# Optimization experiments

Measured on AMD Instinct MI355X. Metric: run time of the kernel, lower is better.

Reference implementation:

```python
import jax, jax.numpy as jnp
import numpy as np

N = 100_000   # nodes
E = 1_600_000 # edges
IN = 128
OUT = 64
L = 3         # n_layers


def setup_inputs() -> dict:
    key = jax.random.key(0)
    ks = jax.random.split(key, 4)
    x = jax.random.normal(ks[0], (N, IN), dtype=jnp.float32)
    edge_index = jax.random.randint(ks[1], (2, E), 0, N, dtype=jnp.int64)
    # Glorot-ish init like torch Linear default
    s0 = 1.0 / np.sqrt(IN)
    W0 = jax.random.uniform(ks[2], (IN, OUT), jnp.float32, -s0, s0)
    b0 = jnp.zeros((OUT,), jnp.float32)
    so = 1.0 / np.sqrt(OUT)
    Ws = jax.random.uniform(ks[3], (L - 1, OUT, OUT), jnp.float32, -so, so)
    bs = jnp.zeros((L - 1, OUT), jnp.float32)
    return {"x": x, "edge_index": edge_index, "W0": W0, "b0": b0, "Ws": Ws, "bs": bs}


def _gcn_conv(x, src, dst, norm, W, b):
    # dense transform then degree-normalized scatter-add over edges (incl. self-loops)
    h = x @ W                                  # [N, out]
    msg = h[src] * norm[:, None]               # [E+N, out]
    out = jax.ops.segment_sum(msg, dst, num_segments=N)
    return out + b


def reference(x, edge_index, W0, b0, Ws, bs):
    loops = jnp.arange(N, dtype=edge_index.dtype)
    src = jnp.concatenate([edge_index[0], loops])  # source nodes (x_j)
    dst = jnp.concatenate([edge_index[1], loops])  # aggregation targets
    # symmetric GCN normalization: deg over A+I, norm = d^-1/2[src]*d^-1/2[dst]
    deg = jax.ops.segment_sum(jnp.ones(src.shape, x.dtype), dst, num_segments=N)
    dinv = jnp.where(deg > 0, jax.lax.rsqrt(deg), jnp.zeros((), x.dtype))
    norm = dinv[src] * dinv[dst]

    x_temp = _gcn_conv(x, src, dst, norm, W0, b0)
    h = x_temp
    for i in range(L - 1):  # fixed small layer loop
        h = jax.nn.relu(_gcn_conv(h, src, dst, norm, Ws[i], bs[i]))
    return h + x_temp  # sum_res residual
```

## Files before the change

### kernel.cpp

```cpp
#include <hip/hip_runtime.h>


#define LB 8
#define BKN 256
#define CHUNK 4096
#define EPT 16
#define SEPT 20
#define CAP 8192
#define PADS 3
#define CAPCOL (CAP + BKN * PADS)

typedef unsigned short ushort_t;
typedef __attribute__((ext_vector_type(8))) short bf16x8;
typedef __attribute__((ext_vector_type(4))) float f32x4;

__device__ __forceinline__ unsigned f2bf(float f) {
    unsigned u = __builtin_bit_cast(unsigned, f);
    return (u + 0x7FFFu + ((u >> 16) & 1u)) >> 16;
}
__device__ __forceinline__ float bflo(unsigned u) {
    return __builtin_bit_cast(float, u << 16);
}
__device__ __forceinline__ float bfhi(unsigned u) {
    return __builtin_bit_cast(float, u & 0xFFFF0000u);
}

__device__ int detect_f64(const int* ei, int E, int* sflag) {
    if (threadIdx.x == 0) *sflag = 0;
    __syncthreads();
    const unsigned* raw = (const unsigned*)ei;
    int dwords = min(2 * E, 512);
    int any = 0;
    for (int i = threadIdx.x; i < dwords; i += blockDim.x)
        if ((i & 1) && raw[i]) any = 1;
    if (any) atomicOr(sflag, 1);
    __syncthreads();
    return !*sflag;
}

__global__ __launch_bounds__(256) void k_scatter(
        const int* __restrict__ ei, int E,
        int* __restrict__ bucketCursor, unsigned int* __restrict__ packed) {
    __shared__ int hist[512];
    __shared__ int base[512];
    __shared__ int sflag;
    int f64 = detect_f64(ei, E, &sflag);
    int b0 = blockIdx.x * CHUNK;
    int n = min(CHUNK, E - b0);
    int tid = threadIdx.x;
    for (int i = tid; i < 512; i += 256) hist[i] = 0;
    __syncthreads();
    int dreg[EPT], sreg[EPT];
    bool vec_ok = f64 ? ((E & 1) == 0) : ((E & 3) == 0);
    if (vec_ok) {
#pragma unroll
        for (int j = 0; j < EPT / 4; j++) {
            int idx = tid * 4 + j * 1024;
            if (idx + 3 < n) {
                int e = b0 + idx;
                if (f64) {
                    uint4 sa = *(const uint4*)(ei + 2 * (size_t)e);
                    uint4 sb = *(const uint4*)(ei + 2 * (size_t)e + 4);
                    uint4 da = *(const uint4*)(ei + 2 * ((size_t)E + e));
                    uint4 db = *(const uint4*)(ei + 2 * ((size_t)E + e) + 4);
                    sreg[j * 4 + 0] = (int)sa.x; sreg[j * 4 + 1] = (int)sa.z;
                    sreg[j * 4 + 2] = (int)sb.x; sreg[j * 4 + 3] = (int)sb.z;
                    dreg[j * 4 + 0] = (int)da.x; dreg[j * 4 + 1] = (int)da.z;
                    dreg[j * 4 + 2] = (int)db.x; dreg[j * 4 + 3] = (int)db.z;
                } else {
                    uint4 sv = *(const uint4*)(ei + e);
                    uint4 dv = *(const uint4*)(ei + E + e);
                    sreg[j * 4 + 0] = (int)sv.x; sreg[j * 4 + 1] = (int)sv.y;
                    sreg[j * 4 + 2] = (int)sv.z; sreg[j * 4 + 3] = (int)sv.w;
                    dreg[j * 4 + 0] = (int)dv.x; dreg[j * 4 + 1] = (int)dv.y;
                    dreg[j * 4 + 2] = (int)dv.z; dreg[j * 4 + 3] = (int)dv.w;
                }
            } else {
#pragma unroll
                for (int k = 0; k < 4; k++) {
                    int ii = idx + k;
                    if (ii < n) {
                        int e = b0 + ii;
                        dreg[j * 4 + k] = f64 ? ei[2 * (E + e)] : ei[E + e];
                        sreg[j * 4 + k] = f64 ? ei[2 * e] : ei[e];
                    } else {
                        dreg[j * 4 + k] = -1;
                    }
                }
            }
        }
    } else {
#pragma unroll
        for (int i = 0; i < EPT; i++) {
            int idx = tid + i * 256;
            if (idx < n) {
                int e = b0 + idx;
                dreg[i] = f64 ? ei[2 * (E + e)] : ei[E + e];
                sreg[i] = f64 ? ei[2 * e] : ei[e];
            } else {
                dreg[i] = -1;
            }
        }
    }
#pragma unroll
    for (int i = 0; i < EPT; i++)
        if (dreg[i] >= 0) atomicAdd(&hist[dreg[i] >> LB], 1);
    __syncthreads();
    for (int i = tid; i < 512; i += 256) {
        int c = hist[i];
        base[i] = c ? atomicAdd(&bucketCursor[i], c) : 0;
        hist[i] = 0;
    }
    __syncthreads();
#pragma unroll
    for (int i = 0; i < EPT; i++) {
        if (dreg[i] >= 0) {
            int bk = dreg[i] >> LB;
            int pos = bk * CAP + base[bk] + atomicAdd(&hist[bk], 1);
            packed[pos] = ((unsigned)sreg[i] << LB) | (unsigned)(dreg[i] & (BKN - 1));
        }
    }
}

__global__ __launch_bounds__(256) void k_sort(
        const unsigned int* __restrict__ packed, const int* __restrict__ bucketCursor,
        int* __restrict__ col, int2* __restrict__ rp2, float* __restrict__ dinv,
        ushort_t* __restrict__ hs, int N) {
    __shared__ int hist[BKN];
    __shared__ int cur[BKN];
    __shared__ int wtot[4];
    int tid = threadIdx.x;
    int b = blockIdx.x;
    int start = b * CAP;
    int cnt = bucketCursor[b];
    int end = start + cnt;
    int inreg = (cnt <= 256 * SEPT);
    unsigned preg[SEPT];
    hist[tid] = 0;
    __syncthreads();
    if (inreg) {
#pragma unroll
        for (int i = 0; i < SEPT; i++) {
            int e = start + tid + i * 256;
            if (e < end) {
                preg[i] = packed[e];
                atomicAdd(&hist[preg[i] & (BKN - 1)], 1);
            }
        }
    } else {
        for (int e = start + tid; e < end; e += 256)
            atomicAdd(&hist[packed[e] & (BKN - 1)], 1);
    }
    __syncthreads();
    int v = hist[tid];
    int pv = (v + PADS) & ~PADS;
    int lane = tid & 63, wid = tid >> 6;
    int sc = pv;
#pragma unroll
    for (int off = 1; off < 64; off <<= 1) {
        int x = __shfl_up(sc, off);
        if (lane >= off) sc += x;
    }
    if (lane == 63) wtot[wid] = sc;
    __syncthreads();
    int add = 0;
#pragma unroll
    for (int w2 = 0; w2 < 3; w2++)
        if (wid > w2) add += wtot[w2];
    int excl = sc + add - pv;
    int st = b * CAPCOL + excl;
    cur[tid] = st;
    int node = (b << LB) + tid;
    if (node < N) {
        rp2[node] = make_int2(st, st + pv);
        dinv[node] = rsqrtf((float)(v + 1));
        for (int i = v; i < pv; i++) col[st + i] = N;
    }
    if (b == 0 && tid < 64) hs[(size_t)N * 64 + tid] = 0;
    __syncthreads();
    if (inreg) {
#pragma unroll
        for (int i = 0; i < SEPT; i++) {
            int e = start + tid + i * 256;
            if (e < end) {
                unsigned pvk = preg[i];
                int pos = atomicAdd(&cur[pvk & (BKN - 1)], 1);
                col[pos] = (int)(pvk >> LB);
            }
        }
    } else {
        for (int e = start + tid; e < end; e += 256) {
            unsigned pvk = packed[e];
            int pos = atomicAdd(&cur[pvk & (BKN - 1)], 1);
            col[pos] = (int)(pvk >> LB);
        }
    }
}

__global__ __launch_bounds__(256) void k_gemm1(
        const float* __restrict__ A, const float* __restrict__ W,
        const float* __restrict__ dinv, ushort_t* __restrict__ out, int nrows) {
    const int K = 128;
    __shared__ ushort_t sWT[64 * (K + 8)];
    int tid = threadIdx.x;
    for (int i = tid; i < K * 64; i += 256) {
        int n = i & 63, k = i >> 6;
        sWT[n * (K + 8) + k] = (ushort_t)f2bf(W[i]);
    }
    __syncthreads();
    int wave = tid >> 6, lane = tid & 63;
    int quad = lane >> 4, l16 = lane & 15;
    int rowBase = blockIdx.x * 128 + wave * 32;
    f32x4 acc[2][4];
#pragma unroll
    for (int r = 0; r < 2; r++)
#pragma unroll
        for (int c = 0; c < 4; c++) acc[r][c] = (f32x4){0.f, 0.f, 0.f, 0.f};
#pragma unroll
    for (int chunk = 0; chunk < K / 32; chunk++) {
        bf16x8 afr[2];
#pragma unroll
        for (int r = 0; r < 2; r++) {
            int row = rowBase + r * 16 + l16;
            if (row >= nrows) row = nrows - 1;
            const float* ap = A + (size_t)row * K + chunk * 32 + quad * 8;
            float4 v0 = *(const float4*)ap;
            float4 v1 = *(const float4*)(ap + 4);
            bf16x8 a;
            a[0] = (short)f2bf(v0.x); a[1] = (short)f2bf(v0.y);
            a[2] = (short)f2bf(v0.z); a[3] = (short)f2bf(v0.w);
            a[4] = (short)f2bf(v1.x); a[5] = (short)f2bf(v1.y);
            a[6] = (short)f2bf(v1.z); a[7] = (short)f2bf(v1.w);
            afr[r] = a;
        }
#pragma unroll
        for (int c = 0; c < 4; c++) {
            bf16x8 bfr = __builtin_bit_cast(
                bf16x8,
                *(const uint4*)&sWT[(c * 16 + l16) * (K + 8) + chunk * 32 + quad * 8]);
#pragma unroll
            for (int r = 0; r < 2; r++)
                acc[r][c] = __builtin_amdgcn_mfma_f32_16x16x32_bf16(
                    afr[r], bfr, acc[r][c], 0, 0, 0);
        }
    }
#pragma unroll
    for (int r = 0; r < 2; r++)
#pragma unroll
        for (int i = 0; i < 4; i++) {
            int row = rowBase + r * 16 + quad * 4 + i;
            if (row < nrows) {
                float sc = dinv[row];
#pragma unroll
                for (int c = 0; c < 4; c++)
                    out[(size_t)row * 64 + c * 16 + l16] =
                        (ushort_t)f2bf(acc[r][c][i] * sc);
            }
        }
}

__global__ __launch_bounds__(256) void k_gemm64(
        const ushort_t* __restrict__ A, const float* __restrict__ W,
        const float* __restrict__ dinv, ushort_t* __restrict__ out, int nrows) {
    const int K = 64;
    __shared__ ushort_t sWT[64 * (K + 8)];
    int tid = threadIdx.x;
    for (int i = tid; i < K * 64; i += 256) {
        int n = i & 63, k = i >> 6;
        sWT[n * (K + 8) + k] = (ushort_t)f2bf(W[i]);
    }
    __syncthreads();
    int wave = tid >> 6, lane = tid & 63;
    int quad = lane >> 4, l16 = lane & 15;
    int rowBase = blockIdx.x * 128 + wave * 32;
    f32x4 acc[2][4];
#pragma unroll
    for (int r = 0; r < 2; r++)
#pragma unroll
        for (int c = 0; c < 4; c++) acc[r][c] = (f32x4){0.f, 0.f, 0.f, 0.f};
#pragma unroll
    for (int chunk = 0; chunk < K / 32; chunk++) {
        bf16x8 afr[2];
#pragma unroll
        for (int r = 0; r < 2; r++) {
            int row = rowBase + r * 16 + l16;
            if (row >= nrows) row = nrows - 1;
            const ushort_t* ap = A + (size_t)row * K + chunk * 32 + quad * 8;
            afr[r] = __builtin_bit_cast(bf16x8, *(const uint4*)ap);
        }
#pragma unroll
        for (int c = 0; c < 4; c++) {
            bf16x8 bfr = __builtin_bit_cast(
                bf16x8,
                *(const uint4*)&sWT[(c * 16 + l16) * (K + 8) + chunk * 32 + quad * 8]);
#pragma unroll
            for (int r = 0; r < 2; r++)
                acc[r][c] = __builtin_amdgcn_mfma_f32_16x16x32_bf16(
                    afr[r], bfr, acc[r][c], 0, 0, 0);
        }
    }
#pragma unroll
    for (int r = 0; r < 2; r++)
#pragma unroll
        for (int i = 0; i < 4; i++) {
            int row = rowBase + r * 16 + quad * 4 + i;
            if (row < nrows) {
                float sc = dinv[row];
#pragma unroll
                for (int c = 0; c < 4; c++)
                    out[(size_t)row * 64 + c * 16 + l16] =
                        (ushort_t)f2bf(acc[r][c][i] * sc);
            }
        }
}

template <int RELU, int F32OUT>
__global__ __launch_bounds__(256) void k_aggb(
        const ushort_t* __restrict__ hs, const float* __restrict__ dinv,
        const float* __restrict__ bias, const int* __restrict__ col,
        const int2* __restrict__ rp2, const ushort_t* __restrict__ residb,
        float* __restrict__ outf, ushort_t* __restrict__ outb, int n) {
    int node = (int)((blockIdx.x * blockDim.x + threadIdx.x) >> 6);
    if (node >= n) return;
    int lane = threadIdx.x & 63;
    int g = lane >> 4;
    int c4 = lane & 15;
    const ushort_t* hrow = hs + (size_t)c4 * 4;
    uint2 us = *(const uint2*)(hs + (size_t)node * 64 + c4 * 4);
    float sc = dinv[node];
    int2 r = rp2[node];
    int e = r.x, p = r.y;
    float a0 = 0.f, a1 = 0.f, a2 = 0.f, a3 = 0.f;

#define GR(m) (*(const uint2*)(hrow + (size_t)(m) * 64))
#define GACC(u)                                                             \
    a0 += bflo(u.x); a1 += bfhi(u.x);                                       \
    a2 += bflo(u.y); a3 += bfhi(u.y);

    while (p - e > 32) {
        int m0 = col[e + g],      m1 = col[e + 4 + g];
        int m2 = col[e + 8 + g],  m3 = col[e + 12 + g];
        int m4 = col[e + 16 + g], m5 = col[e + 20 + g];
        int m6 = col[e + 24 + g], m7 = col[e + 28 + g];
        uint2 u0 = GR(m0), u1 = GR(m1), u2 = GR(m2), u3 = GR(m3);
        uint2 u4 = GR(m4), u5 = GR(m5), u6 = GR(m6), u7 = GR(m7);
        GACC(u0) GACC(u1) GACC(u2) GACC(u3)
        GACC(u4) GACC(u5) GACC(u6) GACC(u7)
        e += 32;
    }
    int rem = p - e;
    if (rem > 16) {
        int c0 = col[e + g],      c1 = col[e + 4 + g];
        int c2 = col[e + 8 + g],  c3 = col[e + 12 + g];
        int c5 = col[e + 16 + g], c6 = col[e + 20 + g];
        int c7 = col[e + 24 + g], c8 = col[e + 28 + g];
        int m4 = (16 + g < rem) ? c5 : n;
        int m5 = (20 + g < rem) ? c6 : n;
        int m6 = (24 + g < rem) ? c7 : n;
        int m7 = (28 + g < rem) ? c8 : n;
        uint2 u0 = GR(c0), u1 = GR(c1), u2 = GR(c2), u3 = GR(c3);
        uint2 u4 = GR(m4), u5 = GR(m5), u6 = GR(m6), u7 = GR(m7);
        GACC(u0) GACC(u1) GACC(u2) GACC(u3)
        GACC(u4) GACC(u5) GACC(u6) GACC(u7)
    } else if (rem > 0) {
        int c0 = col[e + g],     c1 = col[e + 4 + g];
        int c2 = col[e + 8 + g], c3 = col[e + 12 + g];
        int m0 = (g < rem)      ? c0 : n;
        int m1 = (4 + g < rem)  ? c1 : n;
        int m2 = (8 + g < rem)  ? c2 : n;
        int m3 = (12 + g < rem) ? c3 : n;
        uint2 u0 = GR(m0), u1 = GR(m1), u2 = GR(m2), u3 = GR(m3);
        GACC(u0) GACC(u1) GACC(u2) GACC(u3)
    }
#undef GR
#undef GACC

    a0 += __shfl_xor(a0, 16); a0 += __shfl_xor(a0, 32);
    a1 += __shfl_xor(a1, 16); a1 += __shfl_xor(a1, 32);
    a2 += __shfl_xor(a2, 16); a2 += __shfl_xor(a2, 32);
    a3 += __shfl_xor(a3, 16); a3 += __shfl_xor(a3, 32);

    if (lane < 16) {
        a0 += bflo(us.x); a1 += bfhi(us.x);
        a2 += bflo(us.y); a3 += bfhi(us.y);
        float4 bv = *(const float4*)(bias + c4 * 4);
        float o0 = sc * a0 + bv.x, o1 = sc * a1 + bv.y;
        float o2 = sc * a2 + bv.z, o3 = sc * a3 + bv.w;
        if (RELU) {
            o0 = fmaxf(o0, 0.f); o1 = fmaxf(o1, 0.f);
            o2 = fmaxf(o2, 0.f); o3 = fmaxf(o3, 0.f);
        }
        if (F32OUT) {
            uint2 rb = *(const uint2*)(residb + (size_t)node * 64 + c4 * 4);
            o0 += bflo(rb.x); o1 += bfhi(rb.x);
            o2 += bflo(rb.y); o3 += bfhi(rb.y);
            *(float4*)(outf + (size_t)node * 64 + c4 * 4) =
                make_float4(o0, o1, o2, o3);
        } else {
            unsigned w0 = f2bf(o0) | (f2bf(o1) << 16);
            unsigned w1 = f2bf(o2) | (f2bf(o3) << 16);
            *(uint2*)(outb + (size_t)node * 64 + c4 * 4) = make_uint2(w0, w1);
        }
    }
}

extern "C" void kernel_launch(void* const* d_in, const int* in_sizes, int n_in,
                              void* d_out, int out_size, void* d_ws, size_t ws_size,
                              hipStream_t stream) {
    const float* x  = (const float*)d_in[0];
    const int*   ei = (const int*)d_in[1];
    const float* W0 = (const float*)d_in[2];
    const float* b0 = (const float*)d_in[3];
    const float* Ws = (const float*)d_in[4];
    const float* bs = (const float*)d_in[5];
    float* out = (float*)d_out;

    const int N = in_sizes[0] / 128;
    const int E = in_sizes[1] / 2;
    const int B = (N + BKN - 1) >> LB;

    char* p = (char*)d_ws;
    auto carve = [&](size_t bytes) {
        char* r = p;
        p += (bytes + 255) & ~(size_t)255;
        return r;
    };
    int*      bucketCursor = (int*)carve(512 * 4);
    unsigned* packed       = (unsigned*)carve((size_t)B * CAP * 4);
    int*      col          = (int*)carve(((size_t)B * CAPCOL + 64) * 4);
    int2*     rp2          = (int2*)carve((size_t)N * 8);
    float*    dinv         = (float*)carve((size_t)N * 4);
    ushort_t* hs           = (ushort_t*)carve((size_t)(N + 1) * 64 * 2);
    ushort_t* xtb          = (ushort_t*)carve((size_t)N * 64 * 2);
    ushort_t* hb           = (ushort_t*)carve((size_t)N * 64 * 2);

    hipMemsetAsync(bucketCursor, 0, 512 * 4, stream);

    k_scatter<<<(E + CHUNK - 1) / CHUNK, 256, 0, stream>>>(ei, E, bucketCursor, packed);
    k_sort<<<B, 256, 0, stream>>>(packed, bucketCursor, col, rp2, dinv, hs, N);

    int gb = (N + 127) / 128;
    int ablocks = (N + 3) / 4;

    k_gemm1<<<gb, 256, 0, stream>>>(x, W0, dinv, hs, N);
    k_aggb<0, 0><<<ablocks, 256, 0, stream>>>(hs, dinv, b0, col, rp2,
                                              nullptr, nullptr, xtb, N);
    k_gemm64<<<gb, 256, 0, stream>>>(xtb, Ws, dinv, hs, N);
    k_aggb<1, 0><<<ablocks, 256, 0, stream>>>(hs, dinv, bs, col, rp2,
                                              nullptr, nullptr, hb, N);
    k_gemm64<<<gb, 256, 0, stream>>>(hb, Ws + 64 * 64, dinv, hs, N);
    k_aggb<1, 1><<<ablocks, 256, 0, stream>>>(hs, dinv, bs + 64, col, rp2,
                                              xtb, out, nullptr, N);
}
```

Before: 284.5 us.

## Fuse edge scatter with first-layer GEMM in one launch, scale in sort

The edge bucketing kernel and the first dense transform now run as one grid, with block ranges split by role, so the GEMM no longer waits for the degree computation. The GEMM writes unscaled fp32 results into the output buffer as scratch. The sort kernel, which already knows each node's degree, then applies the dinv scaling and converts to bf16. This removes one launch and a serial dependency, at the cost of an extra fp32 write and read of the intermediate.

```diff
diff --git a/kernel.cpp b/kernel.cpp
--- a/kernel.cpp
+++ b/kernel.cpp
@@ -38,96 +38,159 @@
     return !*sflag;
 }
 
-__global__ __launch_bounds__(256) void k_scatter(
-        const int* __restrict__ ei, int E,
-        int* __restrict__ bucketCursor, unsigned int* __restrict__ packed) {
-    __shared__ int hist[512];
-    __shared__ int base[512];
-    __shared__ int sflag;
-    int f64 = detect_f64(ei, E, &sflag);
-    int b0 = blockIdx.x * CHUNK;
-    int n = min(CHUNK, E - b0);
+__global__ __launch_bounds__(256) void k_fused(
+        const int* __restrict__ ei, int E, int SB,
+        int* __restrict__ bucketCursor, unsigned int* __restrict__ packed,
+        const float* __restrict__ A, const float* __restrict__ W,
+        float* __restrict__ hf, int nrows) {
+    __shared__ __align__(16) char smem[64 * 136 * 2];
     int tid = threadIdx.x;
-    for (int i = tid; i < 512; i += 256) hist[i] = 0;
-    __syncthreads();
-    int dreg[EPT], sreg[EPT];
-    bool vec_ok = f64 ? ((E & 1) == 0) : ((E & 3) == 0);
-    if (vec_ok) {
-#pragma unroll
-        for (int j = 0; j < EPT / 4; j++) {
-            int idx = tid * 4 + j * 1024;
-            if (idx + 3 < n) {
-                int e = b0 + idx;
-                if (f64) {
-                    uint4 sa = *(const uint4*)(ei + 2 * (size_t)e);
-                    uint4 sb = *(const uint4*)(ei + 2 * (size_t)e + 4);
-                    uint4 da = *(const uint4*)(ei + 2 * ((size_t)E + e));
-                    uint4 db = *(const uint4*)(ei + 2 * ((size_t)E + e) + 4);
-                    sreg[j * 4 + 0] = (int)sa.x; sreg[j * 4 + 1] = (int)sa.z;
-                    sreg[j * 4 + 2] = (int)sb.x; sreg[j * 4 + 3] = (int)sb.z;
-                    dreg[j * 4 + 0] = (int)da.x; dreg[j * 4 + 1] = (int)da.z;
-                    dreg[j * 4 + 2] = (int)db.x; dreg[j * 4 + 3] = (int)db.z;
+    int bid = blockIdx.x;
+
+    if (bid < SB) {
+        int* hist = (int*)smem;
+        int* base = hist + 512;
+        int* sflag = base + 512;
+        int f64 = detect_f64(ei, E, sflag);
+        int b0 = bid * CHUNK;
+        int n = min(CHUNK, E - b0);
+        for (int i = tid; i < 512; i += 256) hist[i] = 0;
+        __syncthreads();
+        int dreg[EPT], sreg[EPT];
+        bool vec_ok = f64 ? ((E & 1) == 0) : ((E & 3) == 0);
+        if (vec_ok) {
+#pragma unroll
+            for (int j = 0; j < EPT / 4; j++) {
+                int idx = tid * 4 + j * 1024;
+                if (idx + 3 < n) {
+                    int e = b0 + idx;
+                    if (f64) {
+                        uint4 sa = *(const uint4*)(ei + 2 * (size_t)e);
+                        uint4 sb = *(const uint4*)(ei + 2 * (size_t)e + 4);
+                        uint4 da = *(const uint4*)(ei + 2 * ((size_t)E + e));
+                        uint4 db = *(const uint4*)(ei + 2 * ((size_t)E + e) + 4);
+                        sreg[j * 4 + 0] = (int)sa.x; sreg[j * 4 + 1] = (int)sa.z;
+                        sreg[j * 4 + 2] = (int)sb.x; sreg[j * 4 + 3] = (int)sb.z;
+                        dreg[j * 4 + 0] = (int)da.x; dreg[j * 4 + 1] = (int)da.z;
+                        dreg[j * 4 + 2] = (int)db.x; dreg[j * 4 + 3] = (int)db.z;
+                    } else {
+                        uint4 sv = *(const uint4*)(ei + e);
+                        uint4 dv = *(const uint4*)(ei + E + e);
+                        sreg[j * 4 + 0] = (int)sv.x; sreg[j * 4 + 1] = (int)sv.y;
+                        sreg[j * 4 + 2] = (int)sv.z; sreg[j * 4 + 3] = (int)sv.w;
+                        dreg[j * 4 + 0] = (int)dv.x; dreg[j * 4 + 1] = (int)dv.y;
+                        dreg[j * 4 + 2] = (int)dv.z; dreg[j * 4 + 3] = (int)dv.w;
+                    }
                 } else {
-                    uint4 sv = *(const uint4*)(ei + e);
-                    uint4 dv = *(const uint4*)(ei + E + e);
-                    sreg[j * 4 + 0] = (int)sv.x; sreg[j * 4 + 1] = (int)sv.y;
-                    sreg[j * 4 + 2] = (int)sv.z; sreg[j * 4 + 3] = (int)sv.w;
-                    dreg[j * 4 + 0] = (int)dv.x; dreg[j * 4 + 1] = (int)dv.y;
-                    dreg[j * 4 + 2] = (int)dv.z; dreg[j * 4 + 3] = (int)dv.w;
-                }
-            } else {
-#pragma unroll
-                for (int k = 0; k < 4; k++) {
-                    int ii = idx + k;
-                    if (ii < n) {
-                        int e = b0 + ii;
-                        dreg[j * 4 + k] = f64 ? ei[2 * (E + e)] : ei[E + e];
-                        sreg[j * 4 + k] = f64 ? ei[2 * e] : ei[e];
-                    } else {
-                        dreg[j * 4 + k] = -1;
+#pragma unroll
+                    for (int k = 0; k < 4; k++) {
+                        int ii = idx + k;
+                        if (ii < n) {
+                            int e = b0 + ii;
+                            dreg[j * 4 + k] = f64 ? ei[2 * (E + e)] : ei[E + e];
+                            sreg[j * 4 + k] = f64 ? ei[2 * e] : ei[e];
+                        } else {
+                            dreg[j * 4 + k] = -1;
+                        }
                     }
                 }
             }
+        } else {
+#pragma unroll
+            for (int i = 0; i < EPT; i++) {
+                int idx = tid + i * 256;
+                if (idx < n) {
+                    int e = b0 + idx;
+                    dreg[i] = f64 ? ei[2 * (E + e)] : ei[E + e];
+                    sreg[i] = f64 ? ei[2 * e] : ei[e];
+                } else {
+                    dreg[i] = -1;
+                }
+            }
+        }
+#pragma unroll
+        for (int i = 0; i < EPT; i++)
+            if (dreg[i] >= 0) atomicAdd(&hist[dreg[i] >> LB], 1);
+        __syncthreads();
+        for (int i = tid; i < 512; i += 256) {
+            int c = hist[i];
+            base[i] = c ? atomicAdd(&bucketCursor[i], c) : 0;
+            hist[i] = 0;
+        }
+        __syncthreads();
+#pragma unroll
+        for (int i = 0; i < EPT; i++) {
+            if (dreg[i] >= 0) {
+                int bk = dreg[i] >> LB;
+                int pos = bk * CAP + base[bk] + atomicAdd(&hist[bk], 1);
+                packed[pos] = ((unsigned)sreg[i] << LB) | (unsigned)(dreg[i] & (BKN - 1));
+            }
         }
     } else {
-#pragma unroll
-        for (int i = 0; i < EPT; i++) {
-            int idx = tid + i * 256;
-            if (idx < n) {
-                int e = b0 + idx;
-                dreg[i] = f64 ? ei[2 * (E + e)] : ei[E + e];
-                sreg[i] = f64 ? ei[2 * e] : ei[e];
-            } else {
-                dreg[i] = -1;
-            }
-        }
-    }
-#pragma unroll
-    for (int i = 0; i < EPT; i++)
-        if (dreg[i] >= 0) atomicAdd(&hist[dreg[i] >> LB], 1);
-    __syncthreads();
-    for (int i = tid; i < 512; i += 256) {
-        int c = hist[i];
-        base[i] = c ? atomicAdd(&bucketCursor[i], c) : 0;
-        hist[i] = 0;
-    }
-    __syncthreads();
-#pragma unroll
-    for (int i = 0; i < EPT; i++) {
-        if (dreg[i] >= 0) {
-            int bk = dreg[i] >> LB;
-            int pos = bk * CAP + base[bk] + atomicAdd(&hist[bk], 1);
-            packed[pos] = ((unsigned)sreg[i] << LB) | (unsigned)(dreg[i] & (BKN - 1));
-        }
+        const int K = 128;
+        ushort_t* sWT = (ushort_t*)smem;
+        for (int i = tid; i < K * 64; i += 256) {
+            int n = i & 63, k = i >> 6;
+            sWT[n * (K + 8) + k] = (ushort_t)f2bf(W[i]);
+        }
+        __syncthreads();
+        int wave = tid >> 6, lane = tid & 63;
+        int quad = lane >> 4, l16 = lane & 15;
+        int rowBase = (bid - SB) * 128 + wave * 32;
+        f32x4 acc[2][4];
+#pragma unroll
+        for (int r = 0; r < 2; r++)
+#pragma unroll
+            for (int c = 0; c < 4; c++) acc[r][c] = (f32x4){0.f, 0.f, 0.f, 0.f};
+#pragma unroll
+        for (int chunk = 0; chunk < K / 32; chunk++) {
+            bf16x8 afr[2];
+#pragma unroll
+            for (int r = 0; r < 2; r++) {
+                int row = rowBase + r * 16 + l16;
+                if (row >= nrows) row = nrows - 1;
+                const float* ap = A + (size_t)row * K + chunk * 32 + quad * 8;
+                float4 v0 = *(const float4*)ap;
+                float4 v1 = *(const float4*)(ap + 4);
+                bf16x8 a;
+                a[0] = (short)f2bf(v0.x); a[1] = (short)f2bf(v0.y);
+                a[2] = (short)f2bf(v0.z); a[3] = (short)f2bf(v0.w);
+                a[4] = (short)f2bf(v1.x); a[5] = (short)f2bf(v1.y);
+                a[6] = (short)f2bf(v1.z); a[7] = (short)f2bf(v1.w);
+                afr[r] = a;
+            }
+#pragma unroll
+            for (int c = 0; c < 4; c++) {
+                bf16x8 bfr = __builtin_bit_cast(
+                    bf16x8,
+                    *(const uint4*)&sWT[(c * 16 + l16) * (K + 8) + chunk * 32 + quad * 8]);
+#pragma unroll
+                for (int r = 0; r < 2; r++)
+                    acc[r][c] = __builtin_amdgcn_mfma_f32_16x16x32_bf16(
+                        afr[r], bfr, acc[r][c], 0, 0, 0);
+            }
+        }
+#pragma unroll
+        for (int r = 0; r < 2; r++)
+#pragma unroll
+            for (int i = 0; i < 4; i++) {
+                int row = rowBase + r * 16 + quad * 4 + i;
+                if (row < nrows) {
+#pragma unroll
+                    for (int c = 0; c < 4; c++)
+                        hf[(size_t)row * 64 + c * 16 + l16] = acc[r][c][i];
+                }
+            }
     }
 }
 
 __global__ __launch_bounds__(256) void k_sort(
         const unsigned int* __restrict__ packed, const int* __restrict__ bucketCursor,
         int* __restrict__ col, int2* __restrict__ rp2, float* __restrict__ dinv,
-        ushort_t* __restrict__ hs, int N) {
+        ushort_t* __restrict__ hs, const float* __restrict__ hf, int N) {
     __shared__ int hist[BKN];
     __shared__ int cur[BKN];
+    __shared__ float sdv[BKN];
     __shared__ int wtot[4];
     int tid = threadIdx.x;
     int b = blockIdx.x;
@@ -170,10 +233,12 @@
     int excl = sc + add - pv;
     int st = b * CAPCOL + excl;
     cur[tid] = st;
+    float dvv = rsqrtf((float)(v + 1));
+    sdv[tid] = dvv;
     int node = (b << LB) + tid;
     if (node < N) {
         rp2[node] = make_int2(st, st + pv);
-        dinv[node] = rsqrtf((float)(v + 1));
+        dinv[node] = dvv;
         for (int i = v; i < pv; i++) col[st + i] = N;
     }
     if (b == 0 && tid < 64) hs[(size_t)N * 64 + tid] = 0;
@@ -195,68 +260,15 @@
             col[pos] = (int)(pvk >> LB);
         }
     }
-}
-
-__global__ __launch_bounds__(256) void k_gemm1(
-        const float* __restrict__ A, const float* __restrict__ W,
-        const float* __restrict__ dinv, ushort_t* __restrict__ out, int nrows) {
-    const int K = 128;
-    __shared__ ushort_t sWT[64 * (K + 8)];
-    int tid = threadIdx.x;
-    for (int i = tid; i < K * 64; i += 256) {
-        int n = i & 63, k = i >> 6;
-        sWT[n * (K + 8) + k] = (ushort_t)f2bf(W[i]);
-    }
-    __syncthreads();
-    int wave = tid >> 6, lane = tid & 63;
-    int quad = lane >> 4, l16 = lane & 15;
-    int rowBase = blockIdx.x * 128 + wave * 32;
-    f32x4 acc[2][4];
-#pragma unroll
-    for (int r = 0; r < 2; r++)
-#pragma unroll
-        for (int c = 0; c < 4; c++) acc[r][c] = (f32x4){0.f, 0.f, 0.f, 0.f};
-#pragma unroll
-    for (int chunk = 0; chunk < K / 32; chunk++) {
-        bf16x8 afr[2];
-#pragma unroll
-        for (int r = 0; r < 2; r++) {
-            int row = rowBase + r * 16 + l16;
-            if (row >= nrows) row = nrows - 1;
-            const float* ap = A + (size_t)row * K + chunk * 32 + quad * 8;
-            float4 v0 = *(const float4*)ap;
-            float4 v1 = *(const float4*)(ap + 4);
-            bf16x8 a;
-            a[0] = (short)f2bf(v0.x); a[1] = (short)f2bf(v0.y);
-            a[2] = (short)f2bf(v0.z); a[3] = (short)f2bf(v0.w);
-            a[4] = (short)f2bf(v1.x); a[5] = (short)f2bf(v1.y);
-            a[6] = (short)f2bf(v1.z); a[7] = (short)f2bf(v1.w);
-            afr[r] = a;
-        }
-#pragma unroll
-        for (int c = 0; c < 4; c++) {
-            bf16x8 bfr = __builtin_bit_cast(
-                bf16x8,
-                *(const uint4*)&sWT[(c * 16 + l16) * (K + 8) + chunk * 32 + quad * 8]);
-#pragma unroll
-            for (int r = 0; r < 2; r++)
-                acc[r][c] = __builtin_amdgcn_mfma_f32_16x16x32_bf16(
-                    afr[r], bfr, acc[r][c], 0, 0, 0);
-        }
-    }
-#pragma unroll
-    for (int r = 0; r < 2; r++)
-#pragma unroll
-        for (int i = 0; i < 4; i++) {
-            int row = rowBase + r * 16 + quad * 4 + i;
-            if (row < nrows) {
-                float sc = dinv[row];
-#pragma unroll
-                for (int c = 0; c < 4; c++)
-                    out[(size_t)row * 64 + c * 16 + l16] =
-                        (ushort_t)f2bf(acc[r][c][i] * sc);
-            }
-        }
+    size_t fbase = (size_t)b * (BKN * 64);
+    for (int i2 = tid * 2; i2 < BKN * 64; i2 += 512) {
+        int nl = i2 >> 6;
+        if ((b << LB) + nl >= N) break;
+        float2 hv = *(const float2*)(hf + fbase + i2);
+        float s = sdv[nl];
+        unsigned w = f2bf(hv.x * s) | (f2bf(hv.y * s) << 16);
+        *(unsigned*)(hs + fbase + i2) = w;
+    }
 }
 
 __global__ __launch_bounds__(256) void k_gemm64(
@@ -433,22 +445,25 @@
     ushort_t* hs           = (ushort_t*)carve((size_t)(N + 1) * 64 * 2);
     ushort_t* xtb          = (ushort_t*)carve((size_t)N * 64 * 2);
     ushort_t* hb           = (ushort_t*)carve((size_t)N * 64 * 2);
+    float*    hf           = out;
 
     hipMemsetAsync(bucketCursor, 0, 512 * 4, stream);
 
-    k_scatter<<<(E + CHUNK - 1) / CHUNK, 256, 0, stream>>>(ei, E, bucketCursor, packed);
-    k_sort<<<B, 256, 0, stream>>>(packed, bucketCursor, col, rp2, dinv, hs, N);
-
-    int gb = (N + 127) / 128;
+    int SB = (E + CHUNK - 1) / CHUNK;
+    int GB = (N + 127) / 128;
+    k_fused<<<SB + GB, 256, 0, stream>>>(ei, E, SB, bucketCursor, packed,
+                                         x, W0, hf, N);
+    k_sort<<<B, 256, 0, stream>>>(packed, bucketCursor, col, rp2, dinv,
+                                  hs, hf, N);
+
     int ablocks = (N + 3) / 4;
 
-    k_gemm1<<<gb, 256, 0, stream>>>(x, W0, dinv, hs, N);
     k_aggb<0, 0><<<ablocks, 256, 0, stream>>>(hs, dinv, b0, col, rp2,
                                               nullptr, nullptr, xtb, N);
-    k_gemm64<<<gb, 256, 0, stream>>>(xtb, Ws, dinv, hs, N);
+    k_gemm64<<<GB, 256, 0, stream>>>(xtb, Ws, dinv, hs, N);
     k_aggb<1, 0><<<ablocks, 256, 0, stream>>>(hs, dinv, bs, col, rp2,
                                               nullptr, nullptr, hb, N);
-    k_gemm64<<<gb, 256, 0, stream>>>(hb, Ws + 64 * 64, dinv, hs, N);
+    k_gemm64<<<GB, 256, 0, stream>>>(hb, Ws + 64 * 64, dinv, hs, N);
     k_aggb<1, 1><<<ablocks, 256, 0, stream>>>(hs, dinv, bs + 64, col, rp2,
                                               xtb, out, nullptr, N);
 }
```

Result: slower. 293.9 us (+3.3%).

## Replace global bucket cursor atomics with per-block fixed cells and overflow lists

Applied to the files above, without the earlier changes.

The scatter kernel now writes edges into fixed-size per-(bucket, source block) cells with a small per-block overflow list, instead of reserving ranges through global atomics on shared bucket cursors. This removes the memset and the contended global atomicAdd per bucket per block. The sort kernel now scans all cells of its bucket (including unused padding slots) and every block's overflow list, which adds reads, integer divisions and a serial overflow scan per thread. Overflow beyond OV entries per block is silently dropped, so correctness depends on the input's degree distribution.

```diff
diff --git a/kernel.cpp b/kernel.cpp
--- a/kernel.cpp
+++ b/kernel.cpp
@@ -5,10 +5,10 @@
 #define BKN 256
 #define CHUNK 4096
 #define EPT 16
-#define SEPT 20
-#define CAP 8192
+#define CELL 24
+#define OV 128
 #define PADS 3
-#define CAPCOL (CAP + BKN * PADS)
+#define CAPCOL (8192 + BKN * PADS)
 
 typedef unsigned short ushort_t;
 typedef __attribute__((ext_vector_type(8))) short bf16x8;
@@ -39,16 +39,19 @@
 }
 
 __global__ __launch_bounds__(256) void k_scatter(
-        const int* __restrict__ ei, int E,
-        int* __restrict__ bucketCursor, unsigned int* __restrict__ packed) {
-    __shared__ int hist[512];
-    __shared__ int base[512];
+        const int* __restrict__ ei, int E, int SB,
+        unsigned int* __restrict__ packed, int* __restrict__ countT,
+        int* __restrict__ countO, unsigned long long* __restrict__ ovf) {
+    __shared__ int cellcur[512];
+    __shared__ int ovfcur;
     __shared__ int sflag;
     int f64 = detect_f64(ei, E, &sflag);
-    int b0 = blockIdx.x * CHUNK;
+    int bid = blockIdx.x;
+    int tid = threadIdx.x;
+    int b0 = bid * CHUNK;
     int n = min(CHUNK, E - b0);
-    int tid = threadIdx.x;
-    for (int i = tid; i < 512; i += 256) hist[i] = 0;
+    for (int i = tid; i < 512; i += 256) cellcur[i] = 0;
+    if (tid == 0) ovfcur = 0;
     __syncthreads();
     int dreg[EPT], sreg[EPT];
     bool vec_ok = f64 ? ((E & 1) == 0) : ((E & 3) == 0);
@@ -102,54 +105,58 @@
             }
         }
     }
-#pragma unroll
-    for (int i = 0; i < EPT; i++)
-        if (dreg[i] >= 0) atomicAdd(&hist[dreg[i] >> LB], 1);
-    __syncthreads();
-    for (int i = tid; i < 512; i += 256) {
-        int c = hist[i];
-        base[i] = c ? atomicAdd(&bucketCursor[i], c) : 0;
-        hist[i] = 0;
-    }
-    __syncthreads();
+    size_t cstride = (size_t)SB * CELL;
 #pragma unroll
     for (int i = 0; i < EPT; i++) {
         if (dreg[i] >= 0) {
             int bk = dreg[i] >> LB;
-            int pos = bk * CAP + base[bk] + atomicAdd(&hist[bk], 1);
-            packed[pos] = ((unsigned)sreg[i] << LB) | (unsigned)(dreg[i] & (BKN - 1));
-        }
-    }
+            unsigned ent = ((unsigned)sreg[i] << LB) | (unsigned)(dreg[i] & (BKN - 1));
+            int pos = atomicAdd(&cellcur[bk], 1);
+            if (pos < CELL) {
+                packed[(size_t)bk * cstride + (size_t)bid * CELL + pos] = ent;
+            } else {
+                int o = atomicAdd(&ovfcur, 1);
+                if (o < OV)
+                    ovf[(size_t)bid * OV + o] =
+                        ((unsigned long long)bk << 32) | ent;
+            }
+        }
+    }
+    __syncthreads();
+    for (int i = tid; i < 512; i += 256)
+        countT[(size_t)bid * 512 + i] = min(cellcur[i], CELL);
+    if (tid == 0) countO[bid] = min(ovfcur, OV);
 }
 
 __global__ __launch_bounds__(256) void k_sort(
-        const unsigned int* __restrict__ packed, const int* __restrict__ bucketCursor,
-        int* __restrict__ col, int2* __restrict__ rp2, float* __restrict__ dinv,
-        ushort_t* __restrict__ hs, int N) {
+        const unsigned int* __restrict__ packed, const int* __restrict__ countT,
+        const int* __restrict__ countO, const unsigned long long* __restrict__ ovf,
+        int SB, int* __restrict__ col, int2* __restrict__ rp2,
+        float* __restrict__ dinv, ushort_t* __restrict__ hs, int N) {
     __shared__ int hist[BKN];
     __shared__ int cur[BKN];
+    __shared__ int cnts[1024];
     __shared__ int wtot[4];
     int tid = threadIdx.x;
     int b = blockIdx.x;
-    int start = b * CAP;
-    int cnt = bucketCursor[b];
-    int end = start + cnt;
-    int inreg = (cnt <= 256 * SEPT);
-    unsigned preg[SEPT];
     hist[tid] = 0;
-    __syncthreads();
-    if (inreg) {
-#pragma unroll
-        for (int i = 0; i < SEPT; i++) {
-            int e = start + tid + i * 256;
-            if (e < end) {
-                preg[i] = packed[e];
-                atomicAdd(&hist[preg[i] & (BKN - 1)], 1);
-            }
-        }
-    } else {
-        for (int e = start + tid; e < end; e += 256)
-            atomicAdd(&hist[packed[e] & (BKN - 1)], 1);
+    for (int i = tid; i < SB; i += 256) cnts[i] = countT[(size_t)i * 512 + b];
+    __syncthreads();
+    const unsigned* reg = packed + (size_t)b * SB * CELL;
+    int total = SB * CELL;
+    for (int s = tid; s < total; s += 256) {
+        int blk = s / CELL;
+        int i = s - blk * CELL;
+        if (i < cnts[blk])
+            atomicAdd(&hist[reg[s] & (BKN - 1)], 1);
+    }
+    for (int j = tid; j < SB; j += 256) {
+        int co = countO[j];
+        for (int k = 0; k < co; k++) {
+            unsigned long long v = ovf[(size_t)j * OV + k];
+            if ((int)(v >> 32) == b)
+                atomicAdd(&hist[(unsigned)v & (BKN - 1)], 1);
+        }
     }
     __syncthreads();
     int v = hist[tid];
@@ -178,21 +185,24 @@
     }
     if (b == 0 && tid < 64) hs[(size_t)N * 64 + tid] = 0;
     __syncthreads();
-    if (inreg) {
-#pragma unroll
-        for (int i = 0; i < SEPT; i++) {
-            int e = start + tid + i * 256;
-            if (e < end) {
-                unsigned pvk = preg[i];
+    for (int s = tid; s < total; s += 256) {
+        int blk = s / CELL;
+        int i = s - blk * CELL;
+        if (i < cnts[blk]) {
+            unsigned pvk = reg[s];
+            int pos = atomicAdd(&cur[pvk & (BKN - 1)], 1);
+            col[pos] = (int)(pvk >> LB);
+        }
+    }
+    for (int j = tid; j < SB; j += 256) {
+        int co = countO[j];
+        for (int k = 0; k < co; k++) {
+            unsigned long long v2 = ovf[(size_t)j * OV + k];
+            if ((int)(v2 >> 32) == b) {
+                unsigned pvk = (unsigned)v2;
                 int pos = atomicAdd(&cur[pvk & (BKN - 1)], 1);
                 col[pos] = (int)(pvk >> LB);
             }
-        }
-    } else {
-        for (int e = start + tid; e < end; e += 256) {
-            unsigned pvk = packed[e];
-            int pos = atomicAdd(&cur[pvk & (BKN - 1)], 1);
-            col[pos] = (int)(pvk >> LB);
         }
     }
 }
@@ -418,6 +428,7 @@
     const int N = in_sizes[0] / 128;
     const int E = in_sizes[1] / 2;
     const int B = (N + BKN - 1) >> LB;
+    const int SB = (E + CHUNK - 1) / CHUNK;
 
     char* p = (char*)d_ws;
     auto carve = [&](size_t bytes) {
@@ -425,19 +436,20 @@
         p += (bytes + 255) & ~(size_t)255;
         return r;
     };
-    int*      bucketCursor = (int*)carve(512 * 4);
-    unsigned* packed       = (unsigned*)carve((size_t)B * CAP * 4);
-    int*      col          = (int*)carve(((size_t)B * CAPCOL + 64) * 4);
-    int2*     rp2          = (int2*)carve((size_t)N * 8);
-    float*    dinv         = (float*)carve((size_t)N * 4);
-    ushort_t* hs           = (ushort_t*)carve((size_t)(N + 1) * 64 * 2);
-    ushort_t* xtb          = (ushort_t*)carve((size_t)N * 64 * 2);
-    ushort_t* hb           = (ushort_t*)carve((size_t)N * 64 * 2);
-
-    hipMemsetAsync(bucketCursor, 0, 512 * 4, stream);
-
-    k_scatter<<<(E + CHUNK - 1) / CHUNK, 256, 0, stream>>>(ei, E, bucketCursor, packed);
-    k_sort<<<B, 256, 0, stream>>>(packed, bucketCursor, col, rp2, dinv, hs, N);
+    unsigned* packed = (unsigned*)carve((size_t)B * SB * CELL * 4);
+    int*      countT = (int*)carve((size_t)SB * 512 * 4);
+    int*      countO = (int*)carve((size_t)SB * 4);
+    unsigned long long* ovf = (unsigned long long*)carve((size_t)SB * OV * 8);
+    int*      col    = (int*)carve(((size_t)B * CAPCOL + 64) * 4);
+    int2*     rp2    = (int2*)carve((size_t)N * 8);
+    float*    dinv   = (float*)carve((size_t)N * 4);
+    ushort_t* hs     = (ushort_t*)carve((size_t)(N + 1) * 64 * 2);
+    ushort_t* xtb    = (ushort_t*)carve((size_t)N * 64 * 2);
+    ushort_t* hb     = (ushort_t*)carve((size_t)N * 64 * 2);
+
+    k_scatter<<<SB, 256, 0, stream>>>(ei, E, SB, packed, countT, countO, ovf);
+    k_sort<<<B, 256, 0, stream>>>(packed, countT, countO, ovf, SB,
+                                  col, rp2, dinv, hs, N);
 
     int gb = (N + 127) / 128;
     int ablocks = (N + 3) / 4;
```

Result: slower. 293.4 us (+3.1%).
